# Performance work log

Measured on AMD Instinct MI355X. Metric: run time of the kernel, lower is better.

The kernel has to match this reference:

```python
import jax, jax.numpy as jnp
import numpy as np
from jax import lax

B, T, S = 256, 1024, 96
PAD_IDX, START_IDX = 0, 1
NEG = -9999.0


def setup_inputs() -> dict:
    key = jax.random.key(0)
    k1, k2, k3 = jax.random.split(key, 3)
    features = jax.random.normal(k1, (B, T, S), dtype=jnp.float32)
    states = jax.random.randint(k2, (B, T), 0, S, dtype=jnp.int64)
    mask = jnp.ones((B, T), dtype=jnp.float32)
    # transition_matrix init: N(-1, 0.1) then structural masking as in __init__
    transition = -1.0 + 0.1 * jax.random.normal(k3, (S, S), dtype=jnp.float32)
    transition = transition.at[START_IDX, :].set(NEG)
    transition = transition.at[:, PAD_IDX].set(NEG)
    transition = transition.at[PAD_IDX, :].set(NEG)
    transition = transition.at[PAD_IDX, PAD_IDX].set(0.0)
    return {"features": features, "states": states, "mask": mask, "transition": transition}


def reference(features, states, mask, transition):
    # features: [B,T,S] emissions, states: [B,T] gold tags, mask: [B,T] float,
    # transition: [S,S] with transition[i,j] = score(j -> i).
    b, t, s = features.shape

    # ---- numerator: score of the gold path ----
    start = jnp.full((b, 1), START_IDX, dtype=states.dtype)
    states_ext = jnp.concatenate([start, states], axis=1)       # [B,T+1]
    emis = jnp.take_along_axis(features, states[:, :, None], axis=2)[..., 0]  # [B,T]
    trans = transition[states_ext[:, 1:], states_ext[:, :-1]]   # [B,T]
    numerator = jnp.sum((emis + trans) * mask, axis=1)          # [B]

    # ---- denominator: log partition via forward recursion (scan over time) ----
    alpha0 = jnp.full((b, s), NEG, dtype=features.dtype).at[:, START_IDX].set(0.0)

    def step(alpha, xs):
        e_n, m_n = xs  # [B,S], [B]
        # new[b,i] = logsumexp_j(alpha[b,j] + T[i,j]) + emission[b,i]
        new = jax.scipy.special.logsumexp(alpha[:, None, :] + transition[None, :, :], axis=-1) + e_n
        alpha = jnp.where(m_n[:, None] > 0, new, alpha)
        return alpha, None

    alpha, _ = lax.scan(step, alpha0, (jnp.swapaxes(features, 0, 1), mask.T))
    denominator = jax.scipy.special.logsumexp(alpha, axis=-1)   # [B]

    # negative log-likelihood per sequence (standard CRF training objective)
    return denominator - numerator
```

## Files before the change

### kernel.cpp

```cpp
#include <hip/hip_runtime.h>

namespace {
constexpr int kB = 256;
constexpr int kT = 1024;
constexpr int kS = 96;
constexpr int kStart = 1;
constexpr float kCF = 3.5f;
constexpr float kLn2 = 0.69314718055994531f;

constexpr int OFF_PF = 0;
constexpr int OFF_LF = kB * kS;
constexpr int OFF_WB = OFF_LF + kB;
constexpr int OFF_LB = OFF_WB + kB * kS;

__device__ __forceinline__ void renorm96(const float4* pv, float& pnew, float& Lacc) {
  float4 m4 = pv[0];
#pragma unroll
  for (int k = 1; k < 12; ++k) {
    m4.x = fmaxf(m4.x, pv[k].x);
    m4.y = fmaxf(m4.y, pv[k].y);
    m4.z = fmaxf(m4.z, pv[k].z);
    m4.w = fmaxf(m4.w, pv[k].w);
  }
  float m = fmaxf(fmaxf(m4.x, m4.y), fmaxf(m4.z, m4.w));
  m = fmaxf(m, __shfl_xor(m, 1, 64));
  const int e = (__float_as_int(m) >> 23) & 0xFF;
  const float scale = __int_as_float((254 - e) << 23);
  Lacc += (float)(e - 127) * kLn2;
  pnew *= scale;
}

__global__ __launch_bounds__(192) void crf_halves(
    const float* __restrict__ F, const float* __restrict__ mask,
    const float* __restrict__ trans, float* __restrict__ ws) {
  const bool bwd = blockIdx.x >= kB;
  const int b = bwd ? (blockIdx.x - kB) : blockIdx.x;
  const int tid = threadIdx.x;
  const int h = tid & 1;
  const int i = tid >> 1;

  __shared__ __align__(16) float pbuf[2][kS];
  __shared__ __align__(16) float fl[2][16 * kS];
  __shared__ __align__(16) float ml[kT];

  const float* Fb = F + (size_t)b * kT * kS;

  float mw[48];
  if (!bwd) {
    const float4* tp = (const float4*)(trans + i * kS + h * 48);
#pragma unroll
    for (int k = 0; k < 12; ++k) {
      const float4 tv = tp[k];
      mw[4 * k + 0] = __expf(tv.x - kCF);
      mw[4 * k + 1] = __expf(tv.y - kCF);
      mw[4 * k + 2] = __expf(tv.z - kCF);
      mw[4 * k + 3] = __expf(tv.w - kCF);
    }
  } else {
#pragma unroll
    for (int k = 0; k < 48; ++k)
      mw[k] = __expf(trans[(h * 48 + k) * kS + i] - kCF);
  }

  const int gb0 = bwd ? (kT - 16) : 0;
  const int gstep = bwd ? -16 : 16;

  {
    const float4* s = (const float4*)(Fb + (size_t)gb0 * kS + tid * 8);
    const float4 a = s[0], c4 = s[1];
    *(float4*)&fl[0][tid * 8] = a;
    *(float4*)&fl[0][tid * 8 + 4] = c4;
    const float4* mb4 = (const float4*)(mask + (size_t)b * kT);
    for (int idx = tid; idx < kT / 4; idx += 192) ((float4*)ml)[idx] = mb4[idx];
    if (!bwd && h == 0) pbuf[0][i] = (i == kStart) ? 1.0f : 0.0f;
  }
  __syncthreads();

  float Lacc = 0.0f;
  float pown = bwd ? 1.0f : ((i == kStart) ? 1.0f : 0.0f);
  int cur = 0;
  float4 pfa, pfb;

  for (int tc = 0; tc < 32; ++tc) {
    const int fbuf = tc & 1;
    if (tc < 31) {
      const float4* s =
          (const float4*)(Fb + (size_t)(gb0 + (tc + 1) * gstep) * kS + tid * 8);
      pfa = s[0];
      pfb = s[1];
    }
#pragma unroll
    for (int tt = 0; tt < 16; ++tt) {
      const int tl = tc * 16 + tt;
      const int t = bwd ? (kT - 1 - tl) : tl;
      const float f = fl[fbuf][(bwd ? (15 - tt) : tt) * kS + i];
      const float mkv = ml[t];

      if (!bwd) {
        const float* pc = &pbuf[cur][h * 48];
        float4 pv[12];
#pragma unroll
        for (int k = 0; k < 12; ++k) pv[k] = ((const float4*)pc)[k];
        float a0 = 0.f, a1 = 0.f, a2 = 0.f, a3 = 0.f;
#pragma unroll
        for (int k = 0; k < 12; ++k) {
          a0 = fmaf(mw[4 * k + 0], pv[k].x, a0);
          a1 = fmaf(mw[4 * k + 1], pv[k].y, a1);
          a2 = fmaf(mw[4 * k + 2], pv[k].z, a2);
          a3 = fmaf(mw[4 * k + 3], pv[k].w, a3);
        }
        float acc = (a0 + a1) + (a2 + a3);
        acc += __shfl_xor(acc, 1, 64);
        float pnew = (mkv > 0.f) ? acc * __expf(f - kCF) : pown;
        if (((tt + 1) & 7) == 0) renorm96(pv, pnew, Lacc);
        if (tt == 15 && tc < 31) {
          *(float4*)&fl[fbuf ^ 1][tid * 8] = pfa;
          *(float4*)&fl[fbuf ^ 1][tid * 8 + 4] = pfb;
        }
        if (h == 0) pbuf[cur ^ 1][i] = pnew;
        __syncthreads();
        pown = pnew;
      } else {
        const float u = pown * __expf(f - kCF);
        if (h == 0) pbuf[cur ^ 1][i] = u;
        if (tt == 15 && tc < 31) {
          *(float4*)&fl[fbuf ^ 1][tid * 8] = pfa;
          *(float4*)&fl[fbuf ^ 1][tid * 8 + 4] = pfb;
        }
        __syncthreads();
        const float* pc = &pbuf[cur ^ 1][h * 48];
        float4 pv[12];
#pragma unroll
        for (int k = 0; k < 12; ++k) pv[k] = ((const float4*)pc)[k];
        float a0 = 0.f, a1 = 0.f, a2 = 0.f, a3 = 0.f;
#pragma unroll
        for (int k = 0; k < 12; ++k) {
          a0 = fmaf(mw[4 * k + 0], pv[k].x, a0);
          a1 = fmaf(mw[4 * k + 1], pv[k].y, a1);
          a2 = fmaf(mw[4 * k + 2], pv[k].z, a2);
          a3 = fmaf(mw[4 * k + 3], pv[k].w, a3);
        }
        float acc = (a0 + a1) + (a2 + a3);
        acc += __shfl_xor(acc, 1, 64);
        float pnew = (mkv > 0.f) ? acc : pown;
        if (((tt + 1) & 7) == 0) renorm96(pv, pnew, Lacc);
        pown = pnew;
      }
      cur ^= 1;
    }
  }

  if (h == 0) ws[(bwd ? OFF_WB : OFF_PF) + b * kS + i] = pown;
  if (tid == 0) ws[(bwd ? OFF_LB : OFF_LF) + b] = Lacc;
}

__global__ __launch_bounds__(256) void crf_finalize(
    const float* __restrict__ F, const int* __restrict__ states,
    const float* __restrict__ mask, const float* __restrict__ trans,
    const float* __restrict__ ws, float* __restrict__ out) {
  const int b = blockIdx.x;
  const int tid = threadIdx.x;
  const int* st = states + b * kT;
  const float* Fb = F + (size_t)b * kT * kS;
  const float* mb = mask + b * kT;

  float acc = 0.f;
  for (int t = tid; t < kT; t += 256) {
    const int cu = st[t];
    const int pr = (t > 0) ? st[t - 1] : kStart;
    acc += (Fb[(size_t)t * kS + cu] + trans[cu * kS + pr]) * mb[t];
  }
  __shared__ float red[256];
  red[tid] = acc;
  __syncthreads();
  if (tid < 128) red[tid] += red[tid + 128];
  __syncthreads();
  float numv = 0.f;
  if (tid < 64) {
    float v = red[tid] + red[tid + 64];
#pragma unroll
    for (int off = 32; off > 0; off >>= 1) v += __shfl_xor(v, off, 64);
    numv = v;
  }
  __syncthreads();

  float dv = 0.f;
  if (tid < kS) dv = ws[OFF_PF + b * kS + tid] * ws[OFF_WB + b * kS + tid];
  red[tid] = dv;
  __syncthreads();
  if (tid < 128) red[tid] += red[tid + 128];
  __syncthreads();
  if (tid < 64) {
    float v = red[tid] + red[tid + 64];
#pragma unroll
    for (int off = 32; off > 0; off >>= 1) v += __shfl_xor(v, off, 64);
    if (tid == 0)
      out[b] = (ws[OFF_LF + b] + ws[OFF_LB + b] + logf(v)) - numv;
  }
}
}

extern "C" void kernel_launch(void* const* d_in, const int* in_sizes, int n_in,
                              void* d_out, int out_size, void* d_ws, size_t ws_size,
                              hipStream_t stream) {
  const float* F      = (const float*)d_in[0];
  const int*   states = (const int*)d_in[1];
  const float* mask   = (const float*)d_in[2];
  const float* trans  = (const float*)d_in[3];
  float* out = (float*)d_out;
  float* ws  = (float*)d_ws;
  hipLaunchKernelGGL(crf_halves, dim3(2 * kB), dim3(192), 0, stream,
                     F, mask, trans, ws);
  hipLaunchKernelGGL(crf_finalize, dim3(kB), dim3(256), 0, stream,
                     F, states, mask, trans, ws, out);
}
```

Measured before the change: 242.5 us.

## Batch CRF forward/backward chains on MFMA with fp16 pre-exponentiated emissions

Adds a prep kernel that turns emissions into exp(F - c) packed as fp16, writes per-slot mask words into a large workspace, and computes the gold-path numerator. A new chains kernel then advances 16 sequences at once with 16x16x16 fp16 MFMAs against a register-resident exp-transition matrix. Dedicated loader waves stream the emissions into an LDS ring, and the chain state is renormalised by power-of-two scaling every two steps. The aim is to replace the scalar per-sequence FMA recurrence and its per-step block barriers with matrix-core work. In exchange it uses only 32 blocks, relies on fp16 range and precision, and needs a workspace of about 55 MB, falling back to the old path if that is not available.

```diff
diff --git a/kernel.cpp b/kernel.cpp
--- a/kernel.cpp
+++ b/kernel.cpp
@@ -1,26 +1,270 @@
 #include <hip/hip_runtime.h>
 
+typedef unsigned int u32;
+typedef _Float16 h2v __attribute__((ext_vector_type(2)));
+typedef _Float16 h4v __attribute__((ext_vector_type(4)));
+typedef float f4v __attribute__((ext_vector_type(4)));
+struct u32x2 { u32 x, y; };
+
 namespace {
-constexpr int kB = 256;
-constexpr int kT = 1024;
-constexpr int kS = 96;
-constexpr int kStart = 1;
+
+constexpr int kB = 256, kT = 1024, kS = 96, kStart = 1;
 constexpr float kCF = 3.5f;
 constexpr float kLn2 = 0.69314718055994531f;
-
-constexpr int OFF_PF = 0;
-constexpr int OFF_LF = kB * kS;
-constexpr int OFF_WB = OFF_LF + kB;
-constexpr int OFF_LB = OFF_WB + kB * kS;
+constexpr int kNT = 16;
+constexpr int kSlotU = 832;
+constexpr int kNSlots = kNT * kT;
+constexpr size_t kEFGu = (size_t)kNSlots * kSlotU;
+constexpr size_t OPF  = kEFGu;
+constexpr size_t OWB  = OPF + (size_t)kB * kS;
+constexpr size_t OLF  = OWB + (size_t)kB * kS;
+constexpr size_t OLB  = OLF + kB;
+constexpr size_t ONUM = OLB + kB;
+constexpr size_t OMS  = ONUM + kB;
+constexpr size_t kNeedBytes = (OMS + kB) * 4;
+
+__device__ __forceinline__ u32 pkmul(u32 a, u32 b) {
+  u32 d; asm("v_pk_mul_f16 %0, %1, %2" : "=v"(d) : "v"(a), "v"(b)); return d;
+}
+__device__ __forceinline__ u32 pkmax(u32 a, u32 b) {
+  u32 d; asm("v_pk_max_f16 %0, %1, %2" : "=v"(d) : "v"(a), "v"(b)); return d;
+}
+__device__ __forceinline__ u32 pkrtz(float a, float b) {
+  return __builtin_bit_cast(u32, __builtin_amdgcn_cvt_pkrtz(a, b));
+}
+__device__ __forceinline__ h4v mkh4(u32 a, u32 b) {
+  u32x2 t{a, b}; return __builtin_bit_cast(h4v, t);
+}
+
+__device__ __forceinline__ void renorm(u32 (&B)[6][2], float& Lacc) {
+  u32 m = B[0][0];
+#pragma unroll
+  for (int kt = 0; kt < 6; ++kt)
+#pragma unroll
+    for (int pr = 0; pr < 2; ++pr)
+      if (kt | pr) m = pkmax(m, B[kt][pr]);
+  m = pkmax(m, (u32)__shfl_xor((int)m, 16, 64));
+  m = pkmax(m, (u32)__shfl_xor((int)m, 32, 64));
+  m = pkmax(m, (m >> 16) | (m << 16));
+  int e = (int)((m >> 10) & 31);
+  e = e < 1 ? 1 : (e > 25 ? 25 : e);
+  u32 sb = (u32)(26 - e) << 10;
+  sb |= sb << 16;
+#pragma unroll
+  for (int kt = 0; kt < 6; ++kt)
+#pragma unroll
+    for (int pr = 0; pr < 2; ++pr) B[kt][pr] = pkmul(B[kt][pr], sb);
+  Lacc += (float)(e - 11) * kLn2;
+}
+
+__global__ __launch_bounds__(256) void crf_prep(
+    const float* __restrict__ F, const int* __restrict__ states,
+    const float* __restrict__ mask, const float* __restrict__ trans,
+    u32* __restrict__ efg, float* __restrict__ ws) {
+  __shared__ float red[256];
+  const int blk = blockIdx.x;
+  const int tid = threadIdx.x;
+  if (blk < kNSlots) {
+    const int bt = blk >> 10, t = blk & 1023;
+    u32* out = efg + (size_t)blk * kSlotU;
+#pragma unroll
+    for (int qq = 0; qq < 4; ++qq) {
+      const int c = qq * 256 + tid;
+      if (c < 768) {
+        const int ll = c / 12, j = c % 12;
+        const int col = ll & 15, q4 = (ll >> 4) * 4;
+        const int s0 = (j >> 1) * 16 + q4 + (j & 1) * 2;
+        const int b = bt * 16 + col;
+        const float2 fv = *(const float2*)(F + ((size_t)b * kT + t) * kS + s0);
+        out[c] = pkrtz(__expf(fv.x - kCF), __expf(fv.y - kCF));
+      } else if (c < kSlotU) {
+        const int col = (c - 768) & 15;
+        out[c] = (mask[(size_t)(bt * 16 + col) * kT + t] > 0.f) ? ~0u : 0u;
+      }
+    }
+    return;
+  }
+  const int b = blk - kNSlots;
+  const int* st = states + b * kT;
+  const float* Fb = F + (size_t)b * kT * kS;
+  const float* mb = mask + b * kT;
+  float acc = 0.f, msum = 0.f;
+  for (int t = tid; t < kT; t += 256) {
+    const int cu = st[t];
+    const int pr = (t > 0) ? st[t - 1] : kStart;
+    const float mk = mb[t];
+    acc += (Fb[(size_t)t * kS + cu] + trans[cu * kS + pr]) * mk;
+    msum += mk;
+  }
+  red[tid] = acc;
+  __syncthreads();
+  if (tid < 128) red[tid] += red[tid + 128];
+  __syncthreads();
+  if (tid < 64) {
+    float v = red[tid] + red[tid + 64];
+#pragma unroll
+    for (int off = 32; off > 0; off >>= 1) v += __shfl_xor(v, off, 64);
+    if (tid == 0) ws[ONUM + b] = v;
+  }
+  __syncthreads();
+  red[tid] = msum;
+  __syncthreads();
+  if (tid < 128) red[tid] += red[tid + 128];
+  __syncthreads();
+  if (tid < 64) {
+    float v = red[tid] + red[tid + 64];
+#pragma unroll
+    for (int off = 32; off > 0; off >>= 1) v += __shfl_xor(v, off, 64);
+    if (tid == 0) ws[OMS + b] = v;
+  }
+}
+
+__global__ __launch_bounds__(192, 1) void crf_chains(
+    const u32* __restrict__ efg, const float* __restrict__ trans,
+    float* __restrict__ ws) {
+  const int bid = blockIdx.x;
+  const bool bwd = bid >= kNT;
+  const int bt = bwd ? bid - kNT : bid;
+  const int tid = threadIdx.x, wid = tid >> 6, l = tid & 63;
+  __shared__ u32 ring[24 * kSlotU];
+  const u32* tbase = efg + (size_t)bt * kT * kSlotU;
+
+  if (wid != 0) {
+    const int par = wid - 1;
+    auto loadwin = [&](int w) {
+      for (int j = par; j < 8; j += 2) {
+        const int u = w * 8 + j;
+        const int t = bwd ? (kT - 1 - u) : u;
+        const uint4* src = (const uint4*)(tbase + (size_t)t * kSlotU);
+        uint4* dst = (uint4*)(ring + (u % 24) * kSlotU);
+#pragma unroll
+        for (int qq = 0; qq < 4; ++qq) {
+          const int c = qq * 64 + l;
+          if (c < kSlotU / 4) dst[c] = src[c];
+        }
+      }
+    };
+    loadwin(0); loadwin(1);
+    __syncthreads();
+    for (int k = 0; k < 64; ++k) {
+      if (k + 2 < 64) loadwin(k + 2);
+      __syncthreads();
+    }
+    return;
+  }
+
+  const int r = l & 15, q4 = (l >> 4) * 4;
+  h4v A[6][6];
+#pragma unroll
+  for (int it = 0; it < 6; ++it)
+#pragma unroll
+    for (int kt = 0; kt < 6; ++kt) {
+      float m0, m1, m2, m3;
+      if (!bwd) {
+        const float* tp = trans + (it * 16 + r) * kS + kt * 16 + q4;
+        m0 = tp[0]; m1 = tp[1]; m2 = tp[2]; m3 = tp[3];
+      } else {
+        const float* tp = trans + (kt * 16 + q4) * kS + it * 16 + r;
+        m0 = tp[0]; m1 = tp[kS]; m2 = tp[2 * kS]; m3 = tp[3 * kS];
+      }
+      A[it][kt] = mkh4(pkrtz(__expf(m0 - kCF), __expf(m1 - kCF)),
+                       pkrtz(__expf(m2 - kCF), __expf(m3 - kCF)));
+    }
+
+  u32 B[6][2];
+#pragma unroll
+  for (int kt = 0; kt < 6; ++kt) {
+    B[kt][0] = bwd ? 0x3C003C00u : 0u;
+    B[kt][1] = bwd ? 0x3C003C00u : 0u;
+  }
+  if (!bwd && l < 16) B[0][0] = 0x3C000000u;
+
+  float Lacc = 0.f;
+  __syncthreads();
+
+  const u32* sp = ring + l * 12;
+  uint4 e0 = ((const uint4*)sp)[0], e1 = ((const uint4*)sp)[1], e2 = ((const uint4*)sp)[2];
+  u32 mw = ring[768 + l];
+
+  for (int k = 0; k < 64; ++k) {
+#pragma unroll 2
+    for (int j = 0; j < 8; ++j) {
+      const int u = k * 8 + j;
+      const int un = (u < 511) ? u + 1 : 511;
+      const u32* sn = ring + (un % 24) * kSlotU + l * 12;
+      const uint4 f0 = ((const uint4*)sn)[0];
+      const uint4 f1 = ((const uint4*)sn)[1];
+      const uint4 f2 = ((const uint4*)sn)[2];
+      const u32 mn = ring[(un % 24) * kSlotU + 768 + l];
+      const u32 ef[12] = {e0.x, e0.y, e0.z, e0.w, e1.x, e1.y, e1.z, e1.w,
+                          e2.x, e2.y, e2.z, e2.w};
+
+      u32 Bu[6][2];
+#pragma unroll
+      for (int kt = 0; kt < 6; ++kt)
+#pragma unroll
+        for (int pr = 0; pr < 2; ++pr)
+          Bu[kt][pr] = bwd ? pkmul(B[kt][pr], ef[kt * 2 + pr]) : B[kt][pr];
+
+      f4v C[6];
+#pragma unroll
+      for (int it = 0; it < 6; ++it) C[it] = f4v{0.f, 0.f, 0.f, 0.f};
+#pragma unroll
+      for (int kt = 0; kt < 6; ++kt) {
+        const h4v bk = mkh4(Bu[kt][0], Bu[kt][1]);
+#pragma unroll
+        for (int it = 0; it < 6; ++it)
+          C[it] = __builtin_amdgcn_mfma_f32_16x16x16f16(A[it][kt], bk, C[it], 0, 0, 0);
+      }
+#pragma unroll
+      for (int it = 0; it < 6; ++it)
+#pragma unroll
+        for (int pr = 0; pr < 2; ++pr) {
+          u32 cand = pkrtz(C[it][2 * pr], C[it][2 * pr + 1]);
+          if (!bwd) cand = pkmul(cand, ef[it * 2 + pr]);
+          B[it][pr] = mw ? cand : B[it][pr];
+        }
+      if (u & 1) renorm(B, Lacc);
+      e0 = f0; e1 = f1; e2 = f2; mw = mn;
+    }
+    __syncthreads();
+  }
+
+  float* dst = ws + (bwd ? OWB : OPF) + ((size_t)bt * 16 + (l & 15)) * kS;
+#pragma unroll
+  for (int kt = 0; kt < 6; ++kt)
+#pragma unroll
+    for (int pr = 0; pr < 2; ++pr) {
+      const h2v hv = __builtin_bit_cast(h2v, B[kt][pr]);
+      const int s0 = kt * 16 + q4 + pr * 2;
+      dst[s0] = (float)hv[0];
+      dst[s0 + 1] = (float)hv[1];
+    }
+  if (l < 16) ws[(bwd ? OLB : OLF) + bt * 16 + l] = Lacc;
+}
+
+__global__ __launch_bounds__(64) void crf_fin(
+    const float* __restrict__ ws, float* __restrict__ out) {
+  const int b = blockIdx.x, l = threadIdx.x;
+  float d = ws[OPF + (size_t)b * kS + l] * ws[OWB + (size_t)b * kS + l];
+  if (l < 32) d += ws[OPF + (size_t)b * kS + 64 + l] * ws[OWB + (size_t)b * kS + 64 + l];
+#pragma unroll
+  for (int off = 32; off; off >>= 1) d += __shfl_xor(d, off, 64);
+  if (l == 0)
+    out[b] = (ws[OLF + b] + ws[OLB + b] + logf(d) + 2.f * kCF * ws[OMS + b]) - ws[ONUM + b];
+}
+
+constexpr int FB_PF = 0;
+constexpr int FB_LF = kB * kS;
+constexpr int FB_WB = FB_LF + kB;
+constexpr int FB_LB = FB_WB + kB * kS;
 
 __device__ __forceinline__ void renorm96(const float4* pv, float& pnew, float& Lacc) {
   float4 m4 = pv[0];
 #pragma unroll
   for (int k = 1; k < 12; ++k) {
-    m4.x = fmaxf(m4.x, pv[k].x);
-    m4.y = fmaxf(m4.y, pv[k].y);
-    m4.z = fmaxf(m4.z, pv[k].z);
-    m4.w = fmaxf(m4.w, pv[k].w);
+    m4.x = fmaxf(m4.x, pv[k].x); m4.y = fmaxf(m4.y, pv[k].y);
+    m4.z = fmaxf(m4.z, pv[k].z); m4.w = fmaxf(m4.w, pv[k].w);
   }
   float m = fmaxf(fmaxf(m4.x, m4.y), fmaxf(m4.z, m4.w));
   m = fmaxf(m, __shfl_xor(m, 1, 64));
@@ -30,7 +274,7 @@
   pnew *= scale;
 }
 
-__global__ __launch_bounds__(192) void crf_halves(
+__global__ __launch_bounds__(192) void fb_halves(
     const float* __restrict__ F, const float* __restrict__ mask,
     const float* __restrict__ trans, float* __restrict__ ws) {
   const bool bwd = blockIdx.x >= kB;
@@ -38,33 +282,25 @@
   const int tid = threadIdx.x;
   const int h = tid & 1;
   const int i = tid >> 1;
-
   __shared__ __align__(16) float pbuf[2][kS];
   __shared__ __align__(16) float fl[2][16 * kS];
   __shared__ __align__(16) float ml[kT];
-
   const float* Fb = F + (size_t)b * kT * kS;
-
-  float mw[48];
+  float mwv[48];
   if (!bwd) {
     const float4* tp = (const float4*)(trans + i * kS + h * 48);
 #pragma unroll
     for (int k = 0; k < 12; ++k) {
       const float4 tv = tp[k];
-      mw[4 * k + 0] = __expf(tv.x - kCF);
-      mw[4 * k + 1] = __expf(tv.y - kCF);
-      mw[4 * k + 2] = __expf(tv.z - kCF);
-      mw[4 * k + 3] = __expf(tv.w - kCF);
+      mwv[4 * k + 0] = __expf(tv.x - kCF); mwv[4 * k + 1] = __expf(tv.y - kCF);
+      mwv[4 * k + 2] = __expf(tv.z - kCF); mwv[4 * k + 3] = __expf(tv.w - kCF);
     }
   } else {
 #pragma unroll
-    for (int k = 0; k < 48; ++k)
-      mw[k] = __expf(trans[(h * 48 + k) * kS + i] - kCF);
-  }
-
+    for (int k = 0; k < 48; ++k) mwv[k] = __expf(trans[(h * 48 + k) * kS + i] - kCF);
+  }
   const int gb0 = bwd ? (kT - 16) : 0;
   const int gstep = bwd ? -16 : 16;
-
   {
     const float4* s = (const float4*)(Fb + (size_t)gb0 * kS + tid * 8);
     const float4 a = s[0], c4 = s[1];
@@ -75,19 +311,15 @@
     if (!bwd && h == 0) pbuf[0][i] = (i == kStart) ? 1.0f : 0.0f;
   }
   __syncthreads();
-
   float Lacc = 0.0f;
   float pown = bwd ? 1.0f : ((i == kStart) ? 1.0f : 0.0f);
   int cur = 0;
   float4 pfa, pfb;
-
   for (int tc = 0; tc < 32; ++tc) {
     const int fbuf = tc & 1;
     if (tc < 31) {
-      const float4* s =
-          (const float4*)(Fb + (size_t)(gb0 + (tc + 1) * gstep) * kS + tid * 8);
-      pfa = s[0];
-      pfb = s[1];
+      const float4* s = (const float4*)(Fb + (size_t)(gb0 + (tc + 1) * gstep) * kS + tid * 8);
+      pfa = s[0]; pfb = s[1];
     }
 #pragma unroll
     for (int tt = 0; tt < 16; ++tt) {
@@ -95,7 +327,6 @@
       const int t = bwd ? (kT - 1 - tl) : tl;
       const float f = fl[fbuf][(bwd ? (15 - tt) : tt) * kS + i];
       const float mkv = ml[t];
-
       if (!bwd) {
         const float* pc = &pbuf[cur][h * 48];
         float4 pv[12];
@@ -104,10 +335,8 @@
         float a0 = 0.f, a1 = 0.f, a2 = 0.f, a3 = 0.f;
 #pragma unroll
         for (int k = 0; k < 12; ++k) {
-          a0 = fmaf(mw[4 * k + 0], pv[k].x, a0);
-          a1 = fmaf(mw[4 * k + 1], pv[k].y, a1);
-          a2 = fmaf(mw[4 * k + 2], pv[k].z, a2);
-          a3 = fmaf(mw[4 * k + 3], pv[k].w, a3);
+          a0 = fmaf(mwv[4 * k + 0], pv[k].x, a0); a1 = fmaf(mwv[4 * k + 1], pv[k].y, a1);
+          a2 = fmaf(mwv[4 * k + 2], pv[k].z, a2); a3 = fmaf(mwv[4 * k + 3], pv[k].w, a3);
         }
         float acc = (a0 + a1) + (a2 + a3);
         acc += __shfl_xor(acc, 1, 64);
@@ -121,8 +350,8 @@
         __syncthreads();
         pown = pnew;
       } else {
-        const float u = pown * __expf(f - kCF);
-        if (h == 0) pbuf[cur ^ 1][i] = u;
+        const float uu = pown * __expf(f - kCF);
+        if (h == 0) pbuf[cur ^ 1][i] = uu;
         if (tt == 15 && tc < 31) {
           *(float4*)&fl[fbuf ^ 1][tid * 8] = pfa;
           *(float4*)&fl[fbuf ^ 1][tid * 8 + 4] = pfb;
@@ -135,10 +364,8 @@
         float a0 = 0.f, a1 = 0.f, a2 = 0.f, a3 = 0.f;
 #pragma unroll
         for (int k = 0; k < 12; ++k) {
-          a0 = fmaf(mw[4 * k + 0], pv[k].x, a0);
-          a1 = fmaf(mw[4 * k + 1], pv[k].y, a1);
-          a2 = fmaf(mw[4 * k + 2], pv[k].z, a2);
-          a3 = fmaf(mw[4 * k + 3], pv[k].w, a3);
+          a0 = fmaf(mwv[4 * k + 0], pv[k].x, a0); a1 = fmaf(mwv[4 * k + 1], pv[k].y, a1);
+          a2 = fmaf(mwv[4 * k + 2], pv[k].z, a2); a3 = fmaf(mwv[4 * k + 3], pv[k].w, a3);
         }
         float acc = (a0 + a1) + (a2 + a3);
         acc += __shfl_xor(acc, 1, 64);
@@ -149,12 +376,11 @@
       cur ^= 1;
     }
   }
-
-  if (h == 0) ws[(bwd ? OFF_WB : OFF_PF) + b * kS + i] = pown;
-  if (tid == 0) ws[(bwd ? OFF_LB : OFF_LF) + b] = Lacc;
-}
-
-__global__ __launch_bounds__(256) void crf_finalize(
+  if (h == 0) ws[(bwd ? FB_WB : FB_PF) + b * kS + i] = pown;
+  if (tid == 0) ws[(bwd ? FB_LB : FB_LF) + b] = Lacc;
+}
+
+__global__ __launch_bounds__(256) void fb_finalize(
     const float* __restrict__ F, const int* __restrict__ states,
     const float* __restrict__ mask, const float* __restrict__ trans,
     const float* __restrict__ ws, float* __restrict__ out) {
@@ -163,7 +389,6 @@
   const int* st = states + b * kT;
   const float* Fb = F + (size_t)b * kT * kS;
   const float* mb = mask + b * kT;
-
   float acc = 0.f;
   for (int t = tid; t < kT; t += 256) {
     const int cu = st[t];
@@ -183,9 +408,8 @@
     numv = v;
   }
   __syncthreads();
-
   float dv = 0.f;
-  if (tid < kS) dv = ws[OFF_PF + b * kS + tid] * ws[OFF_WB + b * kS + tid];
+  if (tid < kS) dv = ws[FB_PF + b * kS + tid] * ws[FB_WB + b * kS + tid];
   red[tid] = dv;
   __syncthreads();
   if (tid < 128) red[tid] += red[tid + 128];
@@ -194,10 +418,10 @@
     float v = red[tid] + red[tid + 64];
 #pragma unroll
     for (int off = 32; off > 0; off >>= 1) v += __shfl_xor(v, off, 64);
-    if (tid == 0)
-      out[b] = (ws[OFF_LF + b] + ws[OFF_LB + b] + logf(v)) - numv;
-  }
-}
+    if (tid == 0) out[b] = (ws[FB_LF + b] + ws[FB_LB + b] + logf(v)) - numv;
+  }
+}
+
 }
 
 extern "C" void kernel_launch(void* const* d_in, const int* in_sizes, int n_in,
@@ -208,9 +432,17 @@
   const float* mask   = (const float*)d_in[2];
   const float* trans  = (const float*)d_in[3];
   float* out = (float*)d_out;
-  float* ws  = (float*)d_ws;
-  hipLaunchKernelGGL(crf_halves, dim3(2 * kB), dim3(192), 0, stream,
-                     F, mask, trans, ws);
-  hipLaunchKernelGGL(crf_finalize, dim3(kB), dim3(256), 0, stream,
-                     F, states, mask, trans, ws, out);
-}
+  if (ws_size >= kNeedBytes) {
+    hipLaunchKernelGGL(crf_prep, dim3(kNSlots + kB), dim3(256), 0, stream,
+                       F, states, mask, trans, (u32*)d_ws, (float*)d_ws);
+    hipLaunchKernelGGL(crf_chains, dim3(2 * kNT), dim3(192), 0, stream,
+                       (const u32*)d_ws, trans, (float*)d_ws);
+    hipLaunchKernelGGL(crf_fin, dim3(kB), dim3(64), 0, stream,
+                       (const float*)d_ws, out);
+  } else {
+    float* ws = (float*)d_ws;
+    hipLaunchKernelGGL(fb_halves, dim3(2 * kB), dim3(192), 0, stream, F, mask, trans, ws);
+    hipLaunchKernelGGL(fb_finalize, dim3(kB), dim3(256), 0, stream,
+                       F, states, mask, trans, ws, out);
+  }
+}
```

Measured after the change: 421.1 us. +73.7%, slower.

## Fuse forward and backward CRF recursions into one block sharing a barrier

Applied to the files above, without the earlier changes.

Each block now runs both the forward and backward scaled recursions for one sequence, interleaving the two chains so one __syncthreads per time step serves both. This halves the block count and the total number of barriers, and lets the independent chains hide each other's LDS and shuffle latency. The cost is higher register pressure from two transition weight sets and two prefetch streams. The finalize kernel also sums the mask and adds a 2*kCF*msum term to undo the constant scaling in the log partition, which the previous version appears to have omitted.

```diff
diff --git a/kernel.cpp b/kernel.cpp
--- a/kernel.cpp
+++ b/kernel.cpp
@@ -1,26 +1,21 @@
 #include <hip/hip_runtime.h>
 
 namespace {
-constexpr int kB = 256;
-constexpr int kT = 1024;
-constexpr int kS = 96;
-constexpr int kStart = 1;
+constexpr int kB = 256, kT = 1024, kS = 96, kStart = 1;
 constexpr float kCF = 3.5f;
 constexpr float kLn2 = 0.69314718055994531f;
 
-constexpr int OFF_PF = 0;
-constexpr int OFF_LF = kB * kS;
-constexpr int OFF_WB = OFF_LF + kB;
-constexpr int OFF_LB = OFF_WB + kB * kS;
+constexpr int W_PF = 0;
+constexpr int W_LF = kB * kS;
+constexpr int W_WB = W_LF + kB;
+constexpr int W_LB = W_WB + kB * kS;
 
 __device__ __forceinline__ void renorm96(const float4* pv, float& pnew, float& Lacc) {
   float4 m4 = pv[0];
 #pragma unroll
   for (int k = 1; k < 12; ++k) {
-    m4.x = fmaxf(m4.x, pv[k].x);
-    m4.y = fmaxf(m4.y, pv[k].y);
-    m4.z = fmaxf(m4.z, pv[k].z);
-    m4.w = fmaxf(m4.w, pv[k].w);
+    m4.x = fmaxf(m4.x, pv[k].x); m4.y = fmaxf(m4.y, pv[k].y);
+    m4.z = fmaxf(m4.z, pv[k].z); m4.w = fmaxf(m4.w, pv[k].w);
   }
   float m = fmaxf(fmaxf(m4.x, m4.y), fmaxf(m4.z, m4.w));
   m = fmaxf(m, __shfl_xor(m, 1, 64));
@@ -30,131 +25,140 @@
   pnew *= scale;
 }
 
-__global__ __launch_bounds__(192) void crf_halves(
+__global__ __launch_bounds__(192) void crf_fused(
     const float* __restrict__ F, const float* __restrict__ mask,
     const float* __restrict__ trans, float* __restrict__ ws) {
-  const bool bwd = blockIdx.x >= kB;
-  const int b = bwd ? (blockIdx.x - kB) : blockIdx.x;
+  const int b = blockIdx.x;
   const int tid = threadIdx.x;
   const int h = tid & 1;
   const int i = tid >> 1;
 
-  __shared__ __align__(16) float pbuf[2][kS];
-  __shared__ __align__(16) float fl[2][16 * kS];
+  __shared__ __align__(16) float pF[2][kS];
+  __shared__ __align__(16) float uB[2][kS];
+  __shared__ __align__(16) float flF[2][16 * kS];
+  __shared__ __align__(16) float flB[2][16 * kS];
   __shared__ __align__(16) float ml[kT];
 
   const float* Fb = F + (size_t)b * kT * kS;
 
-  float mw[48];
-  if (!bwd) {
+  float mwF[48], mwB[48];
+  {
     const float4* tp = (const float4*)(trans + i * kS + h * 48);
 #pragma unroll
     for (int k = 0; k < 12; ++k) {
       const float4 tv = tp[k];
-      mw[4 * k + 0] = __expf(tv.x - kCF);
-      mw[4 * k + 1] = __expf(tv.y - kCF);
-      mw[4 * k + 2] = __expf(tv.z - kCF);
-      mw[4 * k + 3] = __expf(tv.w - kCF);
+      mwF[4 * k + 0] = __expf(tv.x - kCF); mwF[4 * k + 1] = __expf(tv.y - kCF);
+      mwF[4 * k + 2] = __expf(tv.z - kCF); mwF[4 * k + 3] = __expf(tv.w - kCF);
     }
-  } else {
-#pragma unroll
-    for (int k = 0; k < 48; ++k)
-      mw[k] = __expf(trans[(h * 48 + k) * kS + i] - kCF);
-  }
-
-  const int gb0 = bwd ? (kT - 16) : 0;
-  const int gstep = bwd ? -16 : 16;
+  }
+#pragma unroll
+  for (int k = 0; k < 48; ++k)
+    mwB[k] = __expf(trans[(h * 48 + k) * kS + i] - kCF);
 
   {
-    const float4* s = (const float4*)(Fb + (size_t)gb0 * kS + tid * 8);
-    const float4 a = s[0], c4 = s[1];
-    *(float4*)&fl[0][tid * 8] = a;
-    *(float4*)&fl[0][tid * 8 + 4] = c4;
+    const float4* sF = (const float4*)(Fb + tid * 8);
+    *(float4*)&flF[0][tid * 8] = sF[0];
+    *(float4*)&flF[0][tid * 8 + 4] = sF[1];
+    const float4* sB = (const float4*)(Fb + (size_t)(kT - 16) * kS + tid * 8);
+    *(float4*)&flB[0][tid * 8] = sB[0];
+    *(float4*)&flB[0][tid * 8 + 4] = sB[1];
     const float4* mb4 = (const float4*)(mask + (size_t)b * kT);
     for (int idx = tid; idx < kT / 4; idx += 192) ((float4*)ml)[idx] = mb4[idx];
-    if (!bwd && h == 0) pbuf[0][i] = (i == kStart) ? 1.0f : 0.0f;
-  }
-  __syncthreads();
-
-  float Lacc = 0.0f;
-  float pown = bwd ? 1.0f : ((i == kStart) ? 1.0f : 0.0f);
+    if (h == 0) pF[0][i] = (i == kStart) ? 1.0f : 0.0f;
+  }
+  __syncthreads();
+
+  float pregF = (i == kStart) ? 1.0f : 0.0f;
+  float pregB = 1.0f;
+  float LF = 0.f, LB = 0.f;
   int cur = 0;
-  float4 pfa, pfb;
+  float4 pfF0, pfF1, pfB0, pfB1;
 
   for (int tc = 0; tc < 32; ++tc) {
     const int fbuf = tc & 1;
     if (tc < 31) {
-      const float4* s =
-          (const float4*)(Fb + (size_t)(gb0 + (tc + 1) * gstep) * kS + tid * 8);
-      pfa = s[0];
-      pfb = s[1];
+      const float4* sF = (const float4*)(Fb + (size_t)(tc + 1) * 16 * kS + tid * 8);
+      pfF0 = sF[0]; pfF1 = sF[1];
+      const float4* sB =
+          (const float4*)(Fb + (size_t)(kT - 16 - (tc + 1) * 16) * kS + tid * 8);
+      pfB0 = sB[0]; pfB1 = sB[1];
     }
 #pragma unroll
     for (int tt = 0; tt < 16; ++tt) {
-      const int tl = tc * 16 + tt;
-      const int t = bwd ? (kT - 1 - tl) : tl;
-      const float f = fl[fbuf][(bwd ? (15 - tt) : tt) * kS + i];
-      const float mkv = ml[t];
-
-      if (!bwd) {
-        const float* pc = &pbuf[cur][h * 48];
-        float4 pv[12];
-#pragma unroll
-        for (int k = 0; k < 12; ++k) pv[k] = ((const float4*)pc)[k];
-        float a0 = 0.f, a1 = 0.f, a2 = 0.f, a3 = 0.f;
-#pragma unroll
-        for (int k = 0; k < 12; ++k) {
-          a0 = fmaf(mw[4 * k + 0], pv[k].x, a0);
-          a1 = fmaf(mw[4 * k + 1], pv[k].y, a1);
-          a2 = fmaf(mw[4 * k + 2], pv[k].z, a2);
-          a3 = fmaf(mw[4 * k + 3], pv[k].w, a3);
-        }
-        float acc = (a0 + a1) + (a2 + a3);
-        acc += __shfl_xor(acc, 1, 64);
-        float pnew = (mkv > 0.f) ? acc * __expf(f - kCF) : pown;
-        if (((tt + 1) & 7) == 0) renorm96(pv, pnew, Lacc);
-        if (tt == 15 && tc < 31) {
-          *(float4*)&fl[fbuf ^ 1][tid * 8] = pfa;
-          *(float4*)&fl[fbuf ^ 1][tid * 8 + 4] = pfb;
-        }
-        if (h == 0) pbuf[cur ^ 1][i] = pnew;
-        __syncthreads();
-        pown = pnew;
-      } else {
-        const float u = pown * __expf(f - kCF);
-        if (h == 0) pbuf[cur ^ 1][i] = u;
-        if (tt == 15 && tc < 31) {
-          *(float4*)&fl[fbuf ^ 1][tid * 8] = pfa;
-          *(float4*)&fl[fbuf ^ 1][tid * 8 + 4] = pfb;
-        }
-        __syncthreads();
-        const float* pc = &pbuf[cur ^ 1][h * 48];
-        float4 pv[12];
-#pragma unroll
-        for (int k = 0; k < 12; ++k) pv[k] = ((const float4*)pc)[k];
-        float a0 = 0.f, a1 = 0.f, a2 = 0.f, a3 = 0.f;
-#pragma unroll
-        for (int k = 0; k < 12; ++k) {
-          a0 = fmaf(mw[4 * k + 0], pv[k].x, a0);
-          a1 = fmaf(mw[4 * k + 1], pv[k].y, a1);
-          a2 = fmaf(mw[4 * k + 2], pv[k].z, a2);
-          a3 = fmaf(mw[4 * k + 3], pv[k].w, a3);
-        }
-        float acc = (a0 + a1) + (a2 + a3);
-        acc += __shfl_xor(acc, 1, 64);
-        float pnew = (mkv > 0.f) ? acc : pown;
-        if (((tt + 1) & 7) == 0) renorm96(pv, pnew, Lacc);
-        pown = pnew;
-      }
-      cur ^= 1;
+      const int k = tc * 16 + tt;
+      const int tb = kT - 1 - k;
+      const int nxt = cur ^ 1;
+
+      const float fB = flB[fbuf][(15 - tt) * kS + i];
+      const float uu = pregB * __expf(fB - kCF);
+      if (h == 0) uB[nxt][i] = uu;
+
+      float4 pvF[12];
+      {
+        const float4* pc = (const float4*)&pF[cur][h * 48];
+#pragma unroll
+        for (int q = 0; q < 12; ++q) pvF[q] = pc[q];
+      }
+      float a0 = 0.f, a1 = 0.f, a2 = 0.f, a3 = 0.f;
+#pragma unroll
+      for (int q = 0; q < 12; ++q) {
+        a0 = fmaf(mwF[4 * q + 0], pvF[q].x, a0);
+        a1 = fmaf(mwF[4 * q + 1], pvF[q].y, a1);
+        a2 = fmaf(mwF[4 * q + 2], pvF[q].z, a2);
+        a3 = fmaf(mwF[4 * q + 3], pvF[q].w, a3);
+      }
+      float accF = (a0 + a1) + (a2 + a3);
+      accF += __shfl_xor(accF, 1, 64);
+      const float fF = flF[fbuf][tt * kS + i];
+      float pnewF = (ml[k] > 0.f) ? accF * __expf(fF - kCF) : pregF;
+      if ((k & 7) == 7) renorm96(pvF, pnewF, LF);
+
+      if (tt == 15 && tc < 31) {
+        *(float4*)&flF[fbuf ^ 1][tid * 8] = pfF0;
+        *(float4*)&flF[fbuf ^ 1][tid * 8 + 4] = pfF1;
+        *(float4*)&flB[fbuf ^ 1][tid * 8] = pfB0;
+        *(float4*)&flB[fbuf ^ 1][tid * 8 + 4] = pfB1;
+      }
+      if (h == 0) pF[nxt][i] = pnewF;
+      pregF = pnewF;
+
+      __syncthreads();
+
+      float4 pvB[12];
+      {
+        const float4* pc = (const float4*)&uB[nxt][h * 48];
+#pragma unroll
+        for (int q = 0; q < 12; ++q) pvB[q] = pc[q];
+      }
+      float b0 = 0.f, b1 = 0.f, b2 = 0.f, b3 = 0.f;
+#pragma unroll
+      for (int q = 0; q < 12; ++q) {
+        b0 = fmaf(mwB[4 * q + 0], pvB[q].x, b0);
+        b1 = fmaf(mwB[4 * q + 1], pvB[q].y, b1);
+        b2 = fmaf(mwB[4 * q + 2], pvB[q].z, b2);
+        b3 = fmaf(mwB[4 * q + 3], pvB[q].w, b3);
+      }
+      float accB = (b0 + b1) + (b2 + b3);
+      accB += __shfl_xor(accB, 1, 64);
+      float pnewB = (ml[tb] > 0.f) ? accB : pregB;
+      if ((k & 7) == 7) renorm96(pvB, pnewB, LB);
+      pregB = pnewB;
+
+      cur = nxt;
     }
   }
 
-  if (h == 0) ws[(bwd ? OFF_WB : OFF_PF) + b * kS + i] = pown;
-  if (tid == 0) ws[(bwd ? OFF_LB : OFF_LF) + b] = Lacc;
-}
-
-__global__ __launch_bounds__(256) void crf_finalize(
+  if (h == 0) {
+    ws[W_PF + b * kS + i] = pregF;
+    ws[W_WB + b * kS + i] = pregB;
+  }
+  if (tid == 0) {
+    ws[W_LF + b] = LF;
+    ws[W_LB + b] = LB;
+  }
+}
+
+__global__ __launch_bounds__(256) void crf_fin2(
     const float* __restrict__ F, const int* __restrict__ states,
     const float* __restrict__ mask, const float* __restrict__ trans,
     const float* __restrict__ ws, float* __restrict__ out) {
@@ -164,29 +168,28 @@
   const float* Fb = F + (size_t)b * kT * kS;
   const float* mb = mask + b * kT;
 
-  float acc = 0.f;
+  float acc = 0.f, msum = 0.f;
   for (int t = tid; t < kT; t += 256) {
     const int cu = st[t];
     const int pr = (t > 0) ? st[t - 1] : kStart;
-    acc += (Fb[(size_t)t * kS + cu] + trans[cu * kS + pr]) * mb[t];
+    const float mk = mb[t];
+    acc += (Fb[(size_t)t * kS + cu] + trans[cu * kS + pr]) * mk;
+    msum += mk;
   }
   __shared__ float red[256];
+  __shared__ float numv_sh, msum_sh;
   red[tid] = acc;
   __syncthreads();
   if (tid < 128) red[tid] += red[tid + 128];
   __syncthreads();
-  float numv = 0.f;
   if (tid < 64) {
     float v = red[tid] + red[tid + 64];
 #pragma unroll
     for (int off = 32; off > 0; off >>= 1) v += __shfl_xor(v, off, 64);
-    numv = v;
-  }
-  __syncthreads();
-
-  float dv = 0.f;
-  if (tid < kS) dv = ws[OFF_PF + b * kS + tid] * ws[OFF_WB + b * kS + tid];
-  red[tid] = dv;
+    if (tid == 0) numv_sh = v;
+  }
+  __syncthreads();
+  red[tid] = msum;
   __syncthreads();
   if (tid < 128) red[tid] += red[tid + 128];
   __syncthreads();
@@ -194,8 +197,22 @@
     float v = red[tid] + red[tid + 64];
 #pragma unroll
     for (int off = 32; off > 0; off >>= 1) v += __shfl_xor(v, off, 64);
+    if (tid == 0) msum_sh = v;
+  }
+  __syncthreads();
+
+  float dv = 0.f;
+  if (tid < kS) dv = ws[W_PF + b * kS + tid] * ws[W_WB + b * kS + tid];
+  red[tid] = dv;
+  __syncthreads();
+  if (tid < 128) red[tid] += red[tid + 128];
+  __syncthreads();
+  if (tid < 64) {
+    float v = red[tid] + red[tid + 64];
+#pragma unroll
+    for (int off = 32; off > 0; off >>= 1) v += __shfl_xor(v, off, 64);
     if (tid == 0)
-      out[b] = (ws[OFF_LF + b] + ws[OFF_LB + b] + logf(v)) - numv;
+      out[b] = (ws[W_LF + b] + ws[W_LB + b] + logf(v) + 2.f * kCF * msum_sh) - numv_sh;
   }
 }
 }
@@ -209,8 +226,8 @@
   const float* trans  = (const float*)d_in[3];
   float* out = (float*)d_out;
   float* ws  = (float*)d_ws;
-  hipLaunchKernelGGL(crf_halves, dim3(2 * kB), dim3(192), 0, stream,
+  hipLaunchKernelGGL(crf_fused, dim3(kB), dim3(192), 0, stream,
                      F, mask, trans, ws);
-  hipLaunchKernelGGL(crf_finalize, dim3(kB), dim3(256), 0, stream,
+  hipLaunchKernelGGL(crf_fin2, dim3(kB), dim3(256), 0, stream,
                      F, states, mask, trans, ws, out);
 }
```

Result: slower. 304.4 us (+25.5%).
